# Kernel optimization log

Hardware: AMD Instinct MI355X
Metric: run time of the kernel (lower is better)

The kernel has to match this reference:

```python
import jax, jax.numpy as jnp
import numpy as np

ATTRACTION_W = 1.0
REPULSION_W = 1.0
MARGIN = 0.3  # hardcoded local `margin = 0.3` in the torch forward


def setup_inputs() -> dict:
    key = jax.random.key(0)
    k1, k2, k3 = jax.random.split(key, 3)
    B, N, D, K = 16, 65536, 32, 512
    beta = jax.random.normal(k1, (B, N, 1), dtype=jnp.float32)
    embed = jax.random.normal(k2, (B, N, D), dtype=jnp.float32)
    # instance id per hit: -1 = background, 0..K-1 = instances
    sid = jax.random.randint(k3, (B, N), -1, K).astype(jnp.int32)
    # first K hits are the condensation points, one per instance
    sid = sid.at[:, :K].set(jnp.arange(K, dtype=jnp.int32)[None, :])
    is_cp = jnp.zeros((B, N), dtype=jnp.int32).at[:, :K].set(1)
    return {"beta": beta, "embed": embed, "slice_id": sid, "is_cp": is_cp, "num_instances": K}


def _per_batch(beta_b, emb_b, sid, iscp, K):
    # beta_b: [N], emb_b: [N, D], sid/iscp: [N]
    N = sid.shape[0]
    cp = iscp == 1
    valid = sid >= 0
    noncp = valid & ~cp  # non-cp signal hits
    pos = cp.sum().astype(jnp.float32)
    neg = jnp.float32(N) - pos  # noncp + background
    pos_w = jax.lax.stop_gradient(neg / (pos + 1e-6))
    w = jnp.where(cp, pos_w, jnp.where(noncp, 1.0, 2.0))
    # weighted BCE-with-logits, reduction='mean'
    x = beta_b
    y = cp.astype(jnp.float32)
    bce = jnp.maximum(x, 0.0) - x * y + jnp.log1p(jnp.exp(-jnp.abs(x)))
    beta_ce = (w * bce).mean()

    # segment id: valid hits -> sid, background -> dummy segment K (dropped)
    seg = jnp.where(valid, sid, K)
    counts = jax.ops.segment_sum(valid.astype(jnp.float32), seg, num_segments=K + 1)[:K]
    inst_exists = counts > 0  # the `unique()` set

    # first cp hit index per instance (sentinel N if instance has no cp)
    idxs = jnp.arange(N)
    first_cp = jax.ops.segment_min(jnp.where(cp & valid, idxs, N), seg, num_segments=K + 1)[:K]
    has_cp = first_cp < N
    safe_cp = jnp.minimum(first_cp, N - 1)
    cp_emb = emb_b[safe_cp]  # [K, D]
    cp_beta = beta_b[safe_cp]  # [K]

    # attraction: sum over instances (with a cp) of mean ||e_hit - e_cp||^2
    sid_c = jnp.clip(sid, 0, K - 1)
    d2 = ((emb_b - cp_emb[sid_c]) ** 2).sum(-1)  # [N]
    d2 = jnp.where(valid, d2, 0.0)
    seg_d2 = jax.ops.segment_sum(d2, seg, num_segments=K + 1)[:K]
    attr = (jnp.where(has_cp & inst_exists, seg_d2 / jnp.maximum(counts, 1.0), 0.0).sum()
            * ATTRACTION_W)

    # ranking: instances with exactly 1 cp and >0 noncp hits
    cp_count = jax.ops.segment_sum((cp & valid).astype(jnp.float32), seg, num_segments=K + 1)[:K]
    ncp_count = jax.ops.segment_sum(noncp.astype(jnp.float32), seg, num_segments=K + 1)[:K]
    r = jax.nn.relu(beta_b + MARGIN - cp_beta[sid_c])
    r = jnp.where(noncp, r, 0.0)
    seg_r = jax.ops.segment_sum(r, seg, num_segments=K + 1)[:K]
    qual = (cp_count == 1.0) & (ncp_count > 0)
    n_unique = inst_exists.sum().astype(jnp.float32)
    ranking = (jnp.where(qual, seg_r / jnp.maximum(ncp_count, 1.0), 0.0).sum()
               / jnp.maximum(n_unique, 1.0))

    beta_loss = beta_ce + 2.0 * ranking

    # repulsion over all cp hits; data has exactly one cp per instance so the
    # cp set equals cp_emb (K points), matching torch's emb_b[cp_idx]
    diff = cp_emb[:, None, :] - cp_emb[None, :, :]  # [K, K, D]
    rep = jnp.exp(-(diff ** 2).sum(-1)).mean() * REPULSION_W

    return beta_loss + attr + rep, beta_loss, attr, rep


def reference(beta, embed, slice_id, is_cp, num_instances):
    K = int(num_instances)
    beta2 = beta[..., 0]  # squeeze(-1)
    loss_b, bl, al, rl = jax.vmap(lambda b, e, s, c: _per_batch(b, e, s, c, K))(
        beta2, embed, slice_id, is_cp)
    return loss_b.mean(), bl.mean(), al.mean(), rl.mean()
```

## Files before the change

### kernel.cpp

```cpp
#include <hip/hip_runtime.h>
#include <math.h>

#define N_HITS 65536
#define K_INST 512
#define MARGIN 0.3f
#define BPB    128
#define HITS_PB (N_HITS / BPB)

__device__ __forceinline__ unsigned short f2bf(float f) {
    unsigned u = __float_as_uint(f);
    return (unsigned short)((u + 0x7FFFu + ((u >> 16) & 1u)) >> 16);
}
__device__ __forceinline__ float bf2f(unsigned short h) {
    return __uint_as_float(((unsigned)h) << 16);
}

__global__ __launch_bounds__(256) void k_scan(
    const int* __restrict__ sid, const int* __restrict__ iscp,
    int* first_cp, int* pos_cnt) {
    int b = blockIdx.y;
    size_t bo = (size_t)b * N_HITS;
    int i = blockIdx.x * 256 + threadIdx.x;
    int stride = gridDim.x * 256;
    for (; i < N_HITS; i += stride) {
        int c = iscp[bo + i];
        if (c == 1) {
            atomicAdd(&pos_cnt[b], 1);
            int s = sid[bo + i];
            if (s >= 0) atomicMin(&first_cp[b * K_INST + s], i);
        }
    }
}

__global__ __launch_bounds__(256) void k_gather(
    const float* __restrict__ beta, const float4* __restrict__ embed4,
    const int* __restrict__ first_cp,
    float* cp_beta, float4* cp_emb4, ushort4* cpb_g, int B) {
    int g = blockIdx.x * 256 + threadIdx.x;
    int total = B * K_INST * 8;
    if (g >= total) return;
    int row = g >> 3, sub = g & 7;
    int b = row / K_INST;
    int fc = first_cp[row];
    int safe = min(fc, N_HITS - 1);
    float4 e = embed4[((size_t)b * N_HITS + safe) * 8 + sub];
    cp_emb4[(size_t)row * 8 + sub] = e;
    ushort4 h;
    h.x = f2bf(e.x); h.y = f2bf(e.y); h.z = f2bf(e.z); h.w = f2bf(e.w);
    cpb_g[(size_t)row * 8 + sub] = h;
    if (sub == 0) cp_beta[row] = beta[b * N_HITS + safe];
}

__global__ __launch_bounds__(256, 3) void k_main(
    const float*  __restrict__ beta,
    const float4* __restrict__ embed4,
    const int*    __restrict__ sid_g, const int* __restrict__ iscp_g,
    const ushort4* __restrict__ cpb_g, const float* __restrict__ cp_beta,
    int* pc_cnt, float* pc_d2, float* pc_r,
    int* cnt_packed, float* seg_d2, float* seg_r,
    float* s_cp, float* s_ncp, float* s_bg, int use_part) {
    __shared__ float l_d2[K_INST];
    __shared__ int   l_cnt[K_INST];
    __shared__ float l_r[K_INST];
    __shared__ float l_cb[K_INST];
    __shared__ short st_s[HITS_PB];
    __shared__ ushort4 l_cpb[K_INST * 9];
    __shared__ float l_red[12];

    int b = blockIdx.y, tid = threadIdx.x;
    size_t bo = (size_t)b * N_HITS;
    int base = blockIdx.x * HITS_PB;

    {
        const ushort4* cpt = cpb_g + (size_t)b * K_INST * 8;
        for (int idx = tid; idx < K_INST * 8; idx += 256) {
            l_cpb[(idx >> 3) * 9 + (idx & 7)] = cpt[idx];
        }
    }
    for (int k = tid; k < K_INST; k += 256) {
        l_cnt[k] = 0; l_r[k] = 0.f; l_d2[k] = 0.f;
        l_cb[k] = cp_beta[b * K_INST + k];
    }
    __syncthreads();

    float a_cp = 0.f, a_ncp = 0.f, a_bg = 0.f;
    {
        int s0 = sid_g[bo + base + tid];
        int s1 = sid_g[bo + base + 256 + tid];
        int c0 = iscp_g[bo + base + tid];
        int c1 = iscp_g[bo + base + 256 + tid];
        float x0 = beta[bo + base + tid];
        float x1 = beta[bo + base + 256 + tid];
        st_s[tid]       = (short)s0;
        st_s[256 + tid] = (short)s1;
#pragma unroll
        for (int h = 0; h < 2; ++h) {
            int s = h ? s1 : s0;
            int c = h ? c1 : c0;
            float x = h ? x1 : x0;
            bool cp = (c == 1), valid = (s >= 0), noncp = valid && !cp;
            float t = __expf(-fabsf(x));
            float bce = fmaxf(x, 0.f) - (cp ? x : 0.f) + __logf(1.f + t);
            if (cp) a_cp += bce; else if (noncp) a_ncp += bce; else a_bg += bce;
            if (valid) {
                atomicAdd(&l_cnt[s], cp ? (1 << 20) : 1);
                if (noncp) {
                    float r = x + MARGIN - l_cb[s];
                    if (r > 0.f) atomicAdd(&l_r[s], r);
                }
            }
        }
    }
    __syncthreads();

    {
        int sub = tid & 7, hgrp = tid >> 3;
        constexpr int NIT = HITS_PB / 32;
        short sarr[NIT];
#pragma unroll
        for (int it = 0; it < NIT; ++it) sarr[it] = st_s[it * 32 + hgrp];
#pragma unroll
        for (int it = 0; it < NIT; ++it) {
            int hit = it * 32 + hgrp;
            float4 e = embed4[(bo + base + hit) * 8 + sub];
            int s = sarr[it];
            ushort4 hh = l_cpb[max(s, 0) * 9 + sub];
            float c0 = bf2f(hh.x), c1 = bf2f(hh.y), c2 = bf2f(hh.z), c3 = bf2f(hh.w);
            float q = e.x * (e.x - 2.f * c0) + e.y * (e.y - 2.f * c1)
                    + e.z * (e.z - 2.f * c2) + e.w * (e.w - 2.f * c3);
            q += __shfl_xor(q, 1);
            q += __shfl_xor(q, 2);
            q += __shfl_xor(q, 4);
            if (sub == 0 && s >= 0) atomicAdd(&l_d2[s], q);
        }
    }

    for (int o = 32; o > 0; o >>= 1) {
        a_cp  += __shfl_down(a_cp, o);
        a_ncp += __shfl_down(a_ncp, o);
        a_bg  += __shfl_down(a_bg, o);
    }
    int wave = tid >> 6;
    if ((tid & 63) == 0) { l_red[wave] = a_cp; l_red[4 + wave] = a_ncp; l_red[8 + wave] = a_bg; }
    __syncthreads();
    if (tid == 0) {
        atomicAdd(&s_cp[b],  l_red[0] + l_red[1] + l_red[2]  + l_red[3]);
        atomicAdd(&s_ncp[b], l_red[4] + l_red[5] + l_red[6]  + l_red[7]);
        atomicAdd(&s_bg[b],  l_red[8] + l_red[9] + l_red[10] + l_red[11]);
    }
    if (use_part) {
        size_t po = ((size_t)b * BPB + blockIdx.x) * K_INST;
        for (int k = tid; k < K_INST; k += 256) {
            pc_cnt[po + k] = l_cnt[k];
            pc_d2[po + k]  = l_d2[k];
            pc_r[po + k]   = l_r[k];
        }
    } else {
        for (int k = tid; k < K_INST; k += 256) {
            int cv = l_cnt[k]; if (cv) atomicAdd(&cnt_packed[b * K_INST + k], cv);
            float dv = l_d2[k]; if (dv != 0.f) atomicAdd(&seg_d2[b * K_INST + k], dv);
            float rv = l_r[k]; if (rv != 0.f) atomicAdd(&seg_r[b * K_INST + k], rv);
        }
    }
}

__global__ __launch_bounds__(256) void k_reduce(
    const int* __restrict__ pc_cnt, const float* __restrict__ pc_d2,
    const float* __restrict__ pc_r,
    int* cnt_packed, float* seg_d2, float* seg_r) {
    __shared__ int   rc[4][64];
    __shared__ float rd[4][64];
    __shared__ float rr[4][64];
    int kl = threadIdx.x & 63, p4 = threadIdx.x >> 6;
    int bin = blockIdx.x * 64 + kl;
    int b = bin / K_INST;
    size_t basep = ((size_t)b * BPB) * K_INST + (bin % K_INST);
    int cs = 0; float ds = 0.f, rs = 0.f;
    for (int p = p4 * (BPB / 4); p < (p4 + 1) * (BPB / 4); ++p) {
        cs += pc_cnt[basep + (size_t)p * K_INST];
        ds += pc_d2[basep + (size_t)p * K_INST];
        rs += pc_r[basep + (size_t)p * K_INST];
    }
    rc[p4][kl] = cs; rd[p4][kl] = ds; rr[p4][kl] = rs;
    __syncthreads();
    if (p4 == 0) {
        cnt_packed[bin] = rc[0][kl] + rc[1][kl] + rc[2][kl] + rc[3][kl];
        seg_d2[bin]     = rd[0][kl] + rd[1][kl] + rd[2][kl] + rd[3][kl];
        seg_r[bin]      = rr[0][kl] + rr[1][kl] + rr[2][kl] + rr[3][kl];
    }
}

__global__ __launch_bounds__(512) void k_tail(
    const float4* __restrict__ cp_emb4, const ushort4* __restrict__ cpb_g,
    const int* __restrict__ cnt_packed, const float* __restrict__ seg_d2,
    const float* __restrict__ seg_r, const int* __restrict__ first_cp,
    const int* __restrict__ pos_cnt, const float* __restrict__ s_cp,
    const float* __restrict__ s_ncp, const float* __restrict__ s_bg,
    float* attr_b, float* rank_b, float* nuniq_b, float* rep_b,
    int* ctr, float* out, int B) {
    int tid = threadIdx.x;
    int nrep = B * 16;

    if ((int)blockIdx.x < nrep) {
        __shared__ float4 tile[32 * 8];
        __shared__ float red[8];
        int b = blockIdx.x >> 4, t2 = blockIdx.x & 15;
        const float4* base = cp_emb4 + (size_t)b * K_INST * 8;
        float4 r0[8];
#pragma unroll
        for (int cc = 0; cc < 8; ++cc) r0[cc] = base[(size_t)tid * 8 + cc];
        if (tid < 256) tile[tid] = base[(size_t)t2 * 256 + tid];
        __syncthreads();
        float acc = 0.f;
        for (int j = 0; j < 32; ++j) {
            float d2 = 0.f;
#pragma unroll
            for (int cc = 0; cc < 8; ++cc) {
                float4 ev = tile[j * 8 + cc];
                float ax = r0[cc].x - ev.x, ay = r0[cc].y - ev.y;
                float az = r0[cc].z - ev.z, aw = r0[cc].w - ev.w;
                d2 += ax * ax + ay * ay + az * az + aw * aw;
            }
            acc += __expf(-d2);
        }
        for (int o = 32; o > 0; o >>= 1) acc += __shfl_down(acc, o);
        if ((tid & 63) == 0) red[tid >> 6] = acc;
        __syncthreads();
        if (tid == 0) {
            float t = 0.f;
            for (int w = 0; w < 8; ++w) t += red[w];
            atomicAdd(&rep_b[b], t);
        }
    } else {
        __shared__ float red2[3][8];
        int b = blockIdx.x - nrep, k = tid;
        int v = cnt_packed[b * K_INST + k];
        int ncp = v & 0xFFFFF, cpc = v >> 20;
        int counts = ncp + cpc;
        int fc = first_cp[b * K_INST + k];
        bool has_cp = fc < N_HITS, exists = counts > 0;
        const ushort4* cq = cpb_g + ((size_t)b * K_INST + k) * 8;
        float s2 = 0.f;
#pragma unroll
        for (int j = 0; j < 8; ++j) {
            ushort4 h = cq[j];
            float c0 = bf2f(h.x), c1 = bf2f(h.y), c2 = bf2f(h.z), c3 = bf2f(h.w);
            s2 += c0 * c0 + c1 * c1 + c2 * c2 + c3 * c3;
        }
        float segd = seg_d2[b * K_INST + k] + (float)counts * s2;
        float attr = (has_cp && exists) ? segd / fmaxf((float)counts, 1.f) : 0.f;
        float rank = (cpc == 1 && ncp > 0) ? seg_r[b * K_INST + k] / fmaxf((float)ncp, 1.f) : 0.f;
        float uq = exists ? 1.f : 0.f;
        for (int o = 32; o > 0; o >>= 1) {
            attr += __shfl_down(attr, o);
            rank += __shfl_down(rank, o);
            uq   += __shfl_down(uq, o);
        }
        if ((k & 63) == 0) { red2[0][k >> 6] = attr; red2[1][k >> 6] = rank; red2[2][k >> 6] = uq; }
        __syncthreads();
        if (k == 0) {
            float a = 0.f, r = 0.f, u = 0.f;
            for (int w = 0; w < 8; ++w) { a += red2[0][w]; r += red2[1][w]; u += red2[2][w]; }
            attr_b[b] = a; rank_b[b] = r; nuniq_b[b] = u;
        }
    }

    __shared__ int is_last;
    __syncthreads();
    if (tid == 0) {
        __threadfence();
        int v = atomicAdd(ctr, 1);
        is_last = (v == (int)gridDim.x - 1);
    }
    __syncthreads();
    if (is_last) {
        __threadfence();
        if (tid < 64) {
            int b = tid;
            float loss = 0.f, bl = 0.f, at = 0.f, rp = 0.f;
            if (b < B) {
                float pos = (float)pos_cnt[b];
                float pw = ((float)N_HITS - pos) / (pos + 1e-6f);
                float bce = (pw * s_cp[b] + s_ncp[b] + 2.f * s_bg[b]) / (float)N_HITS;
                float rank = rank_b[b] / fmaxf(nuniq_b[b], 1.f);
                bl = bce + 2.f * rank;
                at = attr_b[b];
                rp = rep_b[b] / (float)(K_INST * K_INST);
                loss = bl + at + rp;
            }
            for (int o = 32; o > 0; o >>= 1) {
                loss += __shfl_down(loss, o);
                bl   += __shfl_down(bl, o);
                at   += __shfl_down(at, o);
                rp   += __shfl_down(rp, o);
            }
            if (tid == 0) {
                float inv = 1.f / (float)B;
                out[0] = loss * inv;
                out[1] = bl * inv;
                out[2] = at * inv;
                out[3] = rp * inv;
            }
        }
    }
}

extern "C" void kernel_launch(void* const* d_in, const int* in_sizes, int n_in,
                              void* d_out, int out_size, void* d_ws, size_t ws_size,
                              hipStream_t stream) {
    const float*  beta   = (const float*)d_in[0];
    const float*  embed  = (const float*)d_in[1];
    const int*    sid    = (const int*)d_in[2];
    const int*    iscp   = (const int*)d_in[3];
    float* out = (float*)d_out;

    int BN = in_sizes[0];
    int B  = BN / N_HITS;
    int BK = B * K_INST;

    char* ws = (char*)d_ws;
    int*   cnt_packed = (int*)ws;
    float* seg_d2     = (float*)(ws + 4 * (size_t)BK);
    float* seg_r      = (float*)(ws + 8 * (size_t)BK);
    float* scal       = (float*)(ws + 12 * (size_t)BK);
    int*   pos_cnt  = (int*)scal;
    float* s_cp     = scal + 1 * B;
    float* s_ncp    = scal + 2 * B;
    float* s_bg     = scal + 3 * B;
    float* attr_b   = scal + 4 * B;
    float* rank_b   = scal + 5 * B;
    float* nuniq_b  = scal + 6 * B;
    float* rep_b    = scal + 7 * B;
    int*   ctr      = (int*)(scal + 8 * B);
    size_t zbytes = 12 * (size_t)BK + 32 * (size_t)B + 16;
    int*     first_cp = (int*)(ws + zbytes);
    float*   cp_beta  = (float*)(ws + zbytes + 4 * (size_t)BK);
    float4*  cp_emb4  = (float4*)(ws + zbytes + 8 * (size_t)BK);
    ushort4* cpb_g    = (ushort4*)(ws + zbytes + 8 * (size_t)BK + 128 * (size_t)BK);
    char*    partbase = ws + zbytes + 8 * (size_t)BK + 128 * (size_t)BK + 64 * (size_t)BK;
    size_t   psz      = (size_t)B * BPB * K_INST * 4;
    int*     pc_cnt   = (int*)partbase;
    float*   pc_d2    = (float*)(partbase + psz);
    float*   pc_r     = (float*)(partbase + 2 * psz);
    size_t   need     = (size_t)(partbase - ws) + 3 * psz;
    int use_part = (ws_size >= need) ? 1 : 0;

    hipMemsetAsync(ws, 0, zbytes, stream);
    hipMemsetAsync(first_cp, 0x7F, 4 * (size_t)BK, stream);

    k_scan<<<dim3(32, B), 256, 0, stream>>>(sid, iscp, first_cp, pos_cnt);

    k_gather<<<(BK * 8 + 255) / 256, 256, 0, stream>>>(beta, (const float4*)embed,
                                                       first_cp, cp_beta, cp_emb4,
                                                       cpb_g, B);

    k_main<<<dim3(BPB, B), 256, 0, stream>>>(beta, (const float4*)embed, sid, iscp,
                                             (const ushort4*)cpb_g, cp_beta,
                                             pc_cnt, pc_d2, pc_r,
                                             cnt_packed, seg_d2, seg_r,
                                             s_cp, s_ncp, s_bg, use_part);

    if (use_part)
        k_reduce<<<BK / 64, 256, 0, stream>>>(pc_cnt, pc_d2, pc_r,
                                              cnt_packed, seg_d2, seg_r);

    k_tail<<<B * 16 + B, 512, 0, stream>>>(cp_emb4, (const ushort4*)cpb_g,
                                           cnt_packed, seg_d2, seg_r,
                                           first_cp, pos_cnt, s_cp, s_ncp, s_bg,
                                           attr_b, rank_b, nuniq_b, rep_b,
                                           ctr, out, B);
}
```

Measured before the change: 279.7 us.

## Stage fp32 centroids in LDS, batch embed loads, use 512-thread blocks

Replaces the bf16 centroid copy with full fp32 centroids staged in shared memory. The attraction term is now the direct squared difference instead of the expanded form with a tail-side norm correction, so the bf16 conversion and the norm loop in the tail kernel are removed. Blocks grow to 512 threads and cover twice as many hits each (half as many blocks per batch). The embed loop issues eight float4 loads at once before computing, to raise memory-level parallelism. The 64 KB fp32 centroid table raises LDS use per block and may cut occupancy, and the k_reduce kernel indexes partials with BPB, so it must keep working with fewer partials.

```diff
diff --git a/kernel.cpp b/kernel.cpp
--- a/kernel.cpp
+++ b/kernel.cpp
@@ -4,7 +4,8 @@
 #define N_HITS 65536
 #define K_INST 512
 #define MARGIN 0.3f
-#define BPB    128
+#define THREADS 512
+#define BPB    64
 #define HITS_PB (N_HITS / BPB)
 
 __device__ __forceinline__ unsigned short f2bf(float f) {
@@ -35,7 +36,7 @@
 __global__ __launch_bounds__(256) void k_gather(
     const float* __restrict__ beta, const float4* __restrict__ embed4,
     const int* __restrict__ first_cp,
-    float* cp_beta, float4* cp_emb4, ushort4* cpb_g, int B) {
+    float* cp_beta, float4* cp_emb4, int B) {
     int g = blockIdx.x * 256 + threadIdx.x;
     int total = B * K_INST * 8;
     if (g >= total) return;
@@ -45,39 +46,34 @@
     int safe = min(fc, N_HITS - 1);
     float4 e = embed4[((size_t)b * N_HITS + safe) * 8 + sub];
     cp_emb4[(size_t)row * 8 + sub] = e;
-    ushort4 h;
-    h.x = f2bf(e.x); h.y = f2bf(e.y); h.z = f2bf(e.z); h.w = f2bf(e.w);
-    cpb_g[(size_t)row * 8 + sub] = h;
     if (sub == 0) cp_beta[row] = beta[b * N_HITS + safe];
 }
 
-__global__ __launch_bounds__(256, 3) void k_main(
+__global__ __launch_bounds__(THREADS, 4) void k_main(
     const float*  __restrict__ beta,
     const float4* __restrict__ embed4,
     const int*    __restrict__ sid_g, const int* __restrict__ iscp_g,
-    const ushort4* __restrict__ cpb_g, const float* __restrict__ cp_beta,
+    const float4* __restrict__ cp_emb4, const float* __restrict__ cp_beta,
     int* pc_cnt, float* pc_d2, float* pc_r,
     int* cnt_packed, float* seg_d2, float* seg_r,
     float* s_cp, float* s_ncp, float* s_bg, int use_part) {
+    __shared__ float4 l_cp[K_INST * 8];
     __shared__ float l_d2[K_INST];
     __shared__ int   l_cnt[K_INST];
     __shared__ float l_r[K_INST];
     __shared__ float l_cb[K_INST];
     __shared__ short st_s[HITS_PB];
-    __shared__ ushort4 l_cpb[K_INST * 9];
-    __shared__ float l_red[12];
+    __shared__ float l_red[24];
 
     int b = blockIdx.y, tid = threadIdx.x;
     size_t bo = (size_t)b * N_HITS;
     int base = blockIdx.x * HITS_PB;
 
     {
-        const ushort4* cpt = cpb_g + (size_t)b * K_INST * 8;
-        for (int idx = tid; idx < K_INST * 8; idx += 256) {
-            l_cpb[(idx >> 3) * 9 + (idx & 7)] = cpt[idx];
-        }
-    }
-    for (int k = tid; k < K_INST; k += 256) {
+        const float4* cpt = cp_emb4 + (size_t)b * K_INST * 8;
+        for (int idx = tid; idx < K_INST * 8; idx += THREADS) l_cp[idx] = cpt[idx];
+    }
+    for (int k = tid; k < K_INST; k += THREADS) {
         l_cnt[k] = 0; l_r[k] = 0.f; l_d2[k] = 0.f;
         l_cb[k] = cp_beta[b * K_INST + k];
     }
@@ -86,13 +82,13 @@
     float a_cp = 0.f, a_ncp = 0.f, a_bg = 0.f;
     {
         int s0 = sid_g[bo + base + tid];
-        int s1 = sid_g[bo + base + 256 + tid];
+        int s1 = sid_g[bo + base + THREADS + tid];
         int c0 = iscp_g[bo + base + tid];
-        int c1 = iscp_g[bo + base + 256 + tid];
+        int c1 = iscp_g[bo + base + THREADS + tid];
         float x0 = beta[bo + base + tid];
-        float x1 = beta[bo + base + 256 + tid];
-        st_s[tid]       = (short)s0;
-        st_s[256 + tid] = (short)s1;
+        float x1 = beta[bo + base + THREADS + tid];
+        st_s[tid]           = (short)s0;
+        st_s[THREADS + tid] = (short)s1;
 #pragma unroll
         for (int h = 0; h < 2; ++h) {
             int s = h ? s1 : s0;
@@ -115,23 +111,34 @@
 
     {
         int sub = tid & 7, hgrp = tid >> 3;
-        constexpr int NIT = HITS_PB / 32;
+        constexpr int NIT = HITS_PB / 64;
+        size_t ebase = (bo + base + hgrp) * 8 + sub;
         short sarr[NIT];
 #pragma unroll
-        for (int it = 0; it < NIT; ++it) sarr[it] = st_s[it * 32 + hgrp];
-#pragma unroll
-        for (int it = 0; it < NIT; ++it) {
-            int hit = it * 32 + hgrp;
-            float4 e = embed4[(bo + base + hit) * 8 + sub];
-            int s = sarr[it];
-            ushort4 hh = l_cpb[max(s, 0) * 9 + sub];
-            float c0 = bf2f(hh.x), c1 = bf2f(hh.y), c2 = bf2f(hh.z), c3 = bf2f(hh.w);
-            float q = e.x * (e.x - 2.f * c0) + e.y * (e.y - 2.f * c1)
-                    + e.z * (e.z - 2.f * c2) + e.w * (e.w - 2.f * c3);
-            q += __shfl_xor(q, 1);
-            q += __shfl_xor(q, 2);
-            q += __shfl_xor(q, 4);
-            if (sub == 0 && s >= 0) atomicAdd(&l_d2[s], q);
+        for (int it = 0; it < NIT; ++it) sarr[it] = st_s[it * 64 + hgrp];
+#pragma unroll
+        for (int half = 0; half < 2; ++half) {
+            float4 pe[8];
+            float4 pc[8];
+#pragma unroll
+            for (int j = 0; j < 8; ++j) {
+                pe[j] = embed4[ebase + (size_t)(half * 8 + j) * 512];
+            }
+#pragma unroll
+            for (int j = 0; j < 8; ++j) {
+                pc[j] = l_cp[max((int)sarr[half * 8 + j], 0) * 8 + sub];
+            }
+#pragma unroll
+            for (int j = 0; j < 8; ++j) {
+                int s = sarr[half * 8 + j];
+                float dx = pe[j].x - pc[j].x, dy = pe[j].y - pc[j].y;
+                float dz = pe[j].z - pc[j].z, dw = pe[j].w - pc[j].w;
+                float q = dx * dx + dy * dy + dz * dz + dw * dw;
+                q += __shfl_xor(q, 1);
+                q += __shfl_xor(q, 2);
+                q += __shfl_xor(q, 4);
+                if (sub == 0 && s >= 0) atomicAdd(&l_d2[s], q);
+            }
         }
     }
 
@@ -141,22 +148,24 @@
         a_bg  += __shfl_down(a_bg, o);
     }
     int wave = tid >> 6;
-    if ((tid & 63) == 0) { l_red[wave] = a_cp; l_red[4 + wave] = a_ncp; l_red[8 + wave] = a_bg; }
+    if ((tid & 63) == 0) { l_red[wave] = a_cp; l_red[8 + wave] = a_ncp; l_red[16 + wave] = a_bg; }
     __syncthreads();
     if (tid == 0) {
-        atomicAdd(&s_cp[b],  l_red[0] + l_red[1] + l_red[2]  + l_red[3]);
-        atomicAdd(&s_ncp[b], l_red[4] + l_red[5] + l_red[6]  + l_red[7]);
-        atomicAdd(&s_bg[b],  l_red[8] + l_red[9] + l_red[10] + l_red[11]);
+        float t0 = 0.f, t1 = 0.f, t2 = 0.f;
+        for (int w = 0; w < 8; ++w) { t0 += l_red[w]; t1 += l_red[8 + w]; t2 += l_red[16 + w]; }
+        atomicAdd(&s_cp[b],  t0);
+        atomicAdd(&s_ncp[b], t1);
+        atomicAdd(&s_bg[b],  t2);
     }
     if (use_part) {
         size_t po = ((size_t)b * BPB + blockIdx.x) * K_INST;
-        for (int k = tid; k < K_INST; k += 256) {
+        for (int k = tid; k < K_INST; k += THREADS) {
             pc_cnt[po + k] = l_cnt[k];
             pc_d2[po + k]  = l_d2[k];
             pc_r[po + k]   = l_r[k];
         }
     } else {
-        for (int k = tid; k < K_INST; k += 256) {
+        for (int k = tid; k < K_INST; k += THREADS) {
             int cv = l_cnt[k]; if (cv) atomicAdd(&cnt_packed[b * K_INST + k], cv);
             float dv = l_d2[k]; if (dv != 0.f) atomicAdd(&seg_d2[b * K_INST + k], dv);
             float rv = l_r[k]; if (rv != 0.f) atomicAdd(&seg_r[b * K_INST + k], rv);
@@ -191,7 +200,7 @@
 }
 
 __global__ __launch_bounds__(512) void k_tail(
-    const float4* __restrict__ cp_emb4, const ushort4* __restrict__ cpb_g,
+    const float4* __restrict__ cp_emb4,
     const int* __restrict__ cnt_packed, const float* __restrict__ seg_d2,
     const float* __restrict__ seg_r, const int* __restrict__ first_cp,
     const int* __restrict__ pos_cnt, const float* __restrict__ s_cp,
@@ -239,15 +248,7 @@
         int counts = ncp + cpc;
         int fc = first_cp[b * K_INST + k];
         bool has_cp = fc < N_HITS, exists = counts > 0;
-        const ushort4* cq = cpb_g + ((size_t)b * K_INST + k) * 8;
-        float s2 = 0.f;
-#pragma unroll
-        for (int j = 0; j < 8; ++j) {
-            ushort4 h = cq[j];
-            float c0 = bf2f(h.x), c1 = bf2f(h.y), c2 = bf2f(h.z), c3 = bf2f(h.w);
-            s2 += c0 * c0 + c1 * c1 + c2 * c2 + c3 * c3;
-        }
-        float segd = seg_d2[b * K_INST + k] + (float)counts * s2;
+        float segd = seg_d2[b * K_INST + k];
         float attr = (has_cp && exists) ? segd / fmaxf((float)counts, 1.f) : 0.f;
         float rank = (cpc == 1 && ncp > 0) ? seg_r[b * K_INST + k] / fmaxf((float)ncp, 1.f) : 0.f;
         float uq = exists ? 1.f : 0.f;
@@ -336,8 +337,7 @@
     int*     first_cp = (int*)(ws + zbytes);
     float*   cp_beta  = (float*)(ws + zbytes + 4 * (size_t)BK);
     float4*  cp_emb4  = (float4*)(ws + zbytes + 8 * (size_t)BK);
-    ushort4* cpb_g    = (ushort4*)(ws + zbytes + 8 * (size_t)BK + 128 * (size_t)BK);
-    char*    partbase = ws + zbytes + 8 * (size_t)BK + 128 * (size_t)BK + 64 * (size_t)BK;
+    char*    partbase = ws + zbytes + 8 * (size_t)BK + 128 * (size_t)BK;
     size_t   psz      = (size_t)B * BPB * K_INST * 4;
     int*     pc_cnt   = (int*)partbase;
     float*   pc_d2    = (float*)(partbase + psz);
@@ -351,20 +351,19 @@
     k_scan<<<dim3(32, B), 256, 0, stream>>>(sid, iscp, first_cp, pos_cnt);
 
     k_gather<<<(BK * 8 + 255) / 256, 256, 0, stream>>>(beta, (const float4*)embed,
-                                                       first_cp, cp_beta, cp_emb4,
-                                                       cpb_g, B);
-
-    k_main<<<dim3(BPB, B), 256, 0, stream>>>(beta, (const float4*)embed, sid, iscp,
-                                             (const ushort4*)cpb_g, cp_beta,
-                                             pc_cnt, pc_d2, pc_r,
-                                             cnt_packed, seg_d2, seg_r,
-                                             s_cp, s_ncp, s_bg, use_part);
+                                                       first_cp, cp_beta, cp_emb4, B);
+
+    k_main<<<dim3(BPB, B), THREADS, 0, stream>>>(beta, (const float4*)embed, sid, iscp,
+                                                 (const float4*)cp_emb4, cp_beta,
+                                                 pc_cnt, pc_d2, pc_r,
+                                                 cnt_packed, seg_d2, seg_r,
+                                                 s_cp, s_ncp, s_bg, use_part);
 
     if (use_part)
         k_reduce<<<BK / 64, 256, 0, stream>>>(pc_cnt, pc_d2, pc_r,
                                               cnt_packed, seg_d2, seg_r);
 
-    k_tail<<<B * 16 + B, 512, 0, stream>>>(cp_emb4, (const ushort4*)cpb_g,
+    k_tail<<<B * 16 + B, 512, 0, stream>>>((const float4*)cp_emb4,
                                            cnt_packed, seg_d2, seg_r,
                                            first_cp, pos_cnt, s_cp, s_ncp, s_bg,
                                            attr_b, rank_b, nuniq_b, rep_b,
```

Result: faster. 246.3 us (-11.9%).

## Replace LDS-staged segment reduction with direct global atomics and fp32 centroids

Applied to the files above, without the earlier changes.

Removes the shared-memory staging of bf16 condensation-point embeddings and the per-block LDS histograms. k_main now reads fp32 cp embeddings straight from global/L2 and atomically accumulates counts, ranking and squared distances into global per-instance bins. The per-block partial buffers and the k_reduce kernel are deleted, and launch bounds are raised to allow more resident blocks. The aim is to cut LDS setup cost, partial-buffer traffic and one kernel launch. In exchange it adds heavy global atomic contention on only 512 bins per batch, with one atomic per hit for each of counts, distance and ranking.

```diff
diff --git a/kernel.cpp b/kernel.cpp
--- a/kernel.cpp
+++ b/kernel.cpp
@@ -6,14 +6,6 @@
 #define MARGIN 0.3f
 #define BPB    128
 #define HITS_PB (N_HITS / BPB)
-
-__device__ __forceinline__ unsigned short f2bf(float f) {
-    unsigned u = __float_as_uint(f);
-    return (unsigned short)((u + 0x7FFFu + ((u >> 16) & 1u)) >> 16);
-}
-__device__ __forceinline__ float bf2f(unsigned short h) {
-    return __uint_as_float(((unsigned)h) << 16);
-}
 
 __global__ __launch_bounds__(256) void k_scan(
     const int* __restrict__ sid, const int* __restrict__ iscp,
@@ -35,7 +27,7 @@
 __global__ __launch_bounds__(256) void k_gather(
     const float* __restrict__ beta, const float4* __restrict__ embed4,
     const int* __restrict__ first_cp,
-    float* cp_beta, float4* cp_emb4, ushort4* cpb_g, int B) {
+    float* cp_beta, float4* cp_emb4, int B) {
     int g = blockIdx.x * 256 + threadIdx.x;
     int total = B * K_INST * 8;
     if (g >= total) return;
@@ -45,45 +37,24 @@
     int safe = min(fc, N_HITS - 1);
     float4 e = embed4[((size_t)b * N_HITS + safe) * 8 + sub];
     cp_emb4[(size_t)row * 8 + sub] = e;
-    ushort4 h;
-    h.x = f2bf(e.x); h.y = f2bf(e.y); h.z = f2bf(e.z); h.w = f2bf(e.w);
-    cpb_g[(size_t)row * 8 + sub] = h;
     if (sub == 0) cp_beta[row] = beta[b * N_HITS + safe];
 }
 
-__global__ __launch_bounds__(256, 3) void k_main(
+__global__ __launch_bounds__(256, 6) void k_main(
     const float*  __restrict__ beta,
     const float4* __restrict__ embed4,
     const int*    __restrict__ sid_g, const int* __restrict__ iscp_g,
-    const ushort4* __restrict__ cpb_g, const float* __restrict__ cp_beta,
-    int* pc_cnt, float* pc_d2, float* pc_r,
+    const float4* __restrict__ cp_emb4, const float* __restrict__ cp_beta,
     int* cnt_packed, float* seg_d2, float* seg_r,
-    float* s_cp, float* s_ncp, float* s_bg, int use_part) {
-    __shared__ float l_d2[K_INST];
-    __shared__ int   l_cnt[K_INST];
-    __shared__ float l_r[K_INST];
-    __shared__ float l_cb[K_INST];
-    __shared__ short st_s[HITS_PB];
-    __shared__ ushort4 l_cpb[K_INST * 9];
+    float* s_cp, float* s_ncp, float* s_bg) {
     __shared__ float l_red[12];
 
     int b = blockIdx.y, tid = threadIdx.x;
     size_t bo = (size_t)b * N_HITS;
     int base = blockIdx.x * HITS_PB;
 
-    {
-        const ushort4* cpt = cpb_g + (size_t)b * K_INST * 8;
-        for (int idx = tid; idx < K_INST * 8; idx += 256) {
-            l_cpb[(idx >> 3) * 9 + (idx & 7)] = cpt[idx];
-        }
-    }
-    for (int k = tid; k < K_INST; k += 256) {
-        l_cnt[k] = 0; l_r[k] = 0.f; l_d2[k] = 0.f;
-        l_cb[k] = cp_beta[b * K_INST + k];
-    }
-    __syncthreads();
-
     float a_cp = 0.f, a_ncp = 0.f, a_bg = 0.f;
+
     {
         int s0 = sid_g[bo + base + tid];
         int s1 = sid_g[bo + base + 256 + tid];
@@ -91,8 +62,6 @@
         int c1 = iscp_g[bo + base + 256 + tid];
         float x0 = beta[bo + base + tid];
         float x1 = beta[bo + base + 256 + tid];
-        st_s[tid]       = (short)s0;
-        st_s[256 + tid] = (short)s1;
 #pragma unroll
         for (int h = 0; h < 2; ++h) {
             int s = h ? s1 : s0;
@@ -103,35 +72,40 @@
             float bce = fmaxf(x, 0.f) - (cp ? x : 0.f) + __logf(1.f + t);
             if (cp) a_cp += bce; else if (noncp) a_ncp += bce; else a_bg += bce;
             if (valid) {
-                atomicAdd(&l_cnt[s], cp ? (1 << 20) : 1);
+                atomicAdd(&cnt_packed[b * K_INST + s], cp ? (1 << 20) : 1);
                 if (noncp) {
-                    float r = x + MARGIN - l_cb[s];
-                    if (r > 0.f) atomicAdd(&l_r[s], r);
+                    float r = x + MARGIN - cp_beta[b * K_INST + s];
+                    if (r > 0.f) atomicAdd(&seg_r[b * K_INST + s], r);
                 }
             }
         }
     }
-    __syncthreads();
 
     {
         int sub = tid & 7, hgrp = tid >> 3;
-        constexpr int NIT = HITS_PB / 32;
-        short sarr[NIT];
-#pragma unroll
-        for (int it = 0; it < NIT; ++it) sarr[it] = st_s[it * 32 + hgrp];
-#pragma unroll
-        for (int it = 0; it < NIT; ++it) {
-            int hit = it * 32 + hgrp;
-            float4 e = embed4[(bo + base + hit) * 8 + sub];
-            int s = sarr[it];
-            ushort4 hh = l_cpb[max(s, 0) * 9 + sub];
-            float c0 = bf2f(hh.x), c1 = bf2f(hh.y), c2 = bf2f(hh.z), c3 = bf2f(hh.w);
-            float q = e.x * (e.x - 2.f * c0) + e.y * (e.y - 2.f * c1)
-                    + e.z * (e.z - 2.f * c2) + e.w * (e.w - 2.f * c3);
-            q += __shfl_xor(q, 1);
-            q += __shfl_xor(q, 2);
-            q += __shfl_xor(q, 4);
-            if (sub == 0 && s >= 0) atomicAdd(&l_d2[s], q);
+        const float4* cpt = cp_emb4 + (size_t)b * K_INST * 8;
+#pragma unroll
+        for (int g = 0; g < 4; ++g) {
+            float4 e[4];
+            int sv[4];
+#pragma unroll
+            for (int k = 0; k < 4; ++k) {
+                int hit = base + (g * 4 + k) * 32 + hgrp;
+                e[k] = embed4[(bo + hit) * 8 + sub];
+                sv[k] = sid_g[bo + hit];
+            }
+#pragma unroll
+            for (int k = 0; k < 4; ++k) {
+                int s = sv[k];
+                float4 c4 = cpt[(size_t)max(s, 0) * 8 + sub];
+                float dx = e[k].x - c4.x, dy = e[k].y - c4.y;
+                float dz = e[k].z - c4.z, dw = e[k].w - c4.w;
+                float q = dx * dx + dy * dy + dz * dz + dw * dw;
+                q += __shfl_xor(q, 1);
+                q += __shfl_xor(q, 2);
+                q += __shfl_xor(q, 4);
+                if (sub == 0 && s >= 0) atomicAdd(&seg_d2[b * K_INST + s], q);
+            }
         }
     }
 
@@ -148,50 +122,10 @@
         atomicAdd(&s_ncp[b], l_red[4] + l_red[5] + l_red[6]  + l_red[7]);
         atomicAdd(&s_bg[b],  l_red[8] + l_red[9] + l_red[10] + l_red[11]);
     }
-    if (use_part) {
-        size_t po = ((size_t)b * BPB + blockIdx.x) * K_INST;
-        for (int k = tid; k < K_INST; k += 256) {
-            pc_cnt[po + k] = l_cnt[k];
-            pc_d2[po + k]  = l_d2[k];
-            pc_r[po + k]   = l_r[k];
-        }
-    } else {
-        for (int k = tid; k < K_INST; k += 256) {
-            int cv = l_cnt[k]; if (cv) atomicAdd(&cnt_packed[b * K_INST + k], cv);
-            float dv = l_d2[k]; if (dv != 0.f) atomicAdd(&seg_d2[b * K_INST + k], dv);
-            float rv = l_r[k]; if (rv != 0.f) atomicAdd(&seg_r[b * K_INST + k], rv);
-        }
-    }
-}
-
-__global__ __launch_bounds__(256) void k_reduce(
-    const int* __restrict__ pc_cnt, const float* __restrict__ pc_d2,
-    const float* __restrict__ pc_r,
-    int* cnt_packed, float* seg_d2, float* seg_r) {
-    __shared__ int   rc[4][64];
-    __shared__ float rd[4][64];
-    __shared__ float rr[4][64];
-    int kl = threadIdx.x & 63, p4 = threadIdx.x >> 6;
-    int bin = blockIdx.x * 64 + kl;
-    int b = bin / K_INST;
-    size_t basep = ((size_t)b * BPB) * K_INST + (bin % K_INST);
-    int cs = 0; float ds = 0.f, rs = 0.f;
-    for (int p = p4 * (BPB / 4); p < (p4 + 1) * (BPB / 4); ++p) {
-        cs += pc_cnt[basep + (size_t)p * K_INST];
-        ds += pc_d2[basep + (size_t)p * K_INST];
-        rs += pc_r[basep + (size_t)p * K_INST];
-    }
-    rc[p4][kl] = cs; rd[p4][kl] = ds; rr[p4][kl] = rs;
-    __syncthreads();
-    if (p4 == 0) {
-        cnt_packed[bin] = rc[0][kl] + rc[1][kl] + rc[2][kl] + rc[3][kl];
-        seg_d2[bin]     = rd[0][kl] + rd[1][kl] + rd[2][kl] + rd[3][kl];
-        seg_r[bin]      = rr[0][kl] + rr[1][kl] + rr[2][kl] + rr[3][kl];
-    }
 }
 
 __global__ __launch_bounds__(512) void k_tail(
-    const float4* __restrict__ cp_emb4, const ushort4* __restrict__ cpb_g,
+    const float4* __restrict__ cp_emb4,
     const int* __restrict__ cnt_packed, const float* __restrict__ seg_d2,
     const float* __restrict__ seg_r, const int* __restrict__ first_cp,
     const int* __restrict__ pos_cnt, const float* __restrict__ s_cp,
@@ -239,15 +173,7 @@
         int counts = ncp + cpc;
         int fc = first_cp[b * K_INST + k];
         bool has_cp = fc < N_HITS, exists = counts > 0;
-        const ushort4* cq = cpb_g + ((size_t)b * K_INST + k) * 8;
-        float s2 = 0.f;
-#pragma unroll
-        for (int j = 0; j < 8; ++j) {
-            ushort4 h = cq[j];
-            float c0 = bf2f(h.x), c1 = bf2f(h.y), c2 = bf2f(h.z), c3 = bf2f(h.w);
-            s2 += c0 * c0 + c1 * c1 + c2 * c2 + c3 * c3;
-        }
-        float segd = seg_d2[b * K_INST + k] + (float)counts * s2;
+        float segd = seg_d2[b * K_INST + k];
         float attr = (has_cp && exists) ? segd / fmaxf((float)counts, 1.f) : 0.f;
         float rank = (cpc == 1 && ncp > 0) ? seg_r[b * K_INST + k] / fmaxf((float)ncp, 1.f) : 0.f;
         float uq = exists ? 1.f : 0.f;
@@ -336,14 +262,6 @@
     int*     first_cp = (int*)(ws + zbytes);
     float*   cp_beta  = (float*)(ws + zbytes + 4 * (size_t)BK);
     float4*  cp_emb4  = (float4*)(ws + zbytes + 8 * (size_t)BK);
-    ushort4* cpb_g    = (ushort4*)(ws + zbytes + 8 * (size_t)BK + 128 * (size_t)BK);
-    char*    partbase = ws + zbytes + 8 * (size_t)BK + 128 * (size_t)BK + 64 * (size_t)BK;
-    size_t   psz      = (size_t)B * BPB * K_INST * 4;
-    int*     pc_cnt   = (int*)partbase;
-    float*   pc_d2    = (float*)(partbase + psz);
-    float*   pc_r     = (float*)(partbase + 2 * psz);
-    size_t   need     = (size_t)(partbase - ws) + 3 * psz;
-    int use_part = (ws_size >= need) ? 1 : 0;
 
     hipMemsetAsync(ws, 0, zbytes, stream);
     hipMemsetAsync(first_cp, 0x7F, 4 * (size_t)BK, stream);
@@ -351,20 +269,14 @@
     k_scan<<<dim3(32, B), 256, 0, stream>>>(sid, iscp, first_cp, pos_cnt);
 
     k_gather<<<(BK * 8 + 255) / 256, 256, 0, stream>>>(beta, (const float4*)embed,
-                                                       first_cp, cp_beta, cp_emb4,
-                                                       cpb_g, B);
+                                                       first_cp, cp_beta, cp_emb4, B);
 
     k_main<<<dim3(BPB, B), 256, 0, stream>>>(beta, (const float4*)embed, sid, iscp,
-                                             (const ushort4*)cpb_g, cp_beta,
-                                             pc_cnt, pc_d2, pc_r,
+                                             (const float4*)cp_emb4, cp_beta,
                                              cnt_packed, seg_d2, seg_r,
-                                             s_cp, s_ncp, s_bg, use_part);
-
-    if (use_part)
-        k_reduce<<<BK / 64, 256, 0, stream>>>(pc_cnt, pc_d2, pc_r,
-                                              cnt_packed, seg_d2, seg_r);
-
-    k_tail<<<B * 16 + B, 512, 0, stream>>>(cp_emb4, (const ushort4*)cpb_g,
+                                             s_cp, s_ncp, s_bg);
+
+    k_tail<<<B * 16 + B, 512, 0, stream>>>((const float4*)cp_emb4,
                                            cnt_packed, seg_d2, seg_r,
                                            first_cp, pos_cnt, s_cp, s_ncp, s_bg,
                                            attr_b, rank_b, nuniq_b, rep_b,
```

Measured after the change: 351.9 us. 25.8% more time.
